# Kernel optimization log

Measured on AMD Instinct MI355X. Metric: run time of the kernel, lower is better.

Reference implementation:

```python
import jax, jax.numpy as jnp
import numpy as np

DIM = 2048
NUM_HEADS = 16
NUM_KV_HEADS = 4
HEAD_DIM = DIM // NUM_HEADS
KV_DIM = NUM_KV_HEADS * HEAD_DIM
ROPE_BASE = 10000.0
QK_GAIN_INIT = 1.0
BSZ, SEQ = 4, 2048


def rms_norm(x):
    eps = jnp.finfo(x.dtype).eps
    return x * jax.lax.rsqrt(jnp.mean(x * x, axis=-1, keepdims=True) + eps)


def rope_cos_sin(seqlen, head_dim, base, dtype):
    inv_freq = base ** (-jnp.arange(0, head_dim, 2, dtype=jnp.float32) / head_dim)
    t = jnp.arange(seqlen, dtype=jnp.float32)
    freqs = t[:, None] * inv_freq[None, :]  # [S, hd/2]
    return jnp.cos(freqs).astype(dtype), jnp.sin(freqs).astype(dtype)


def apply_rotary(x, cos, sin):
    # x: [B, H, S, hd]; cos/sin: [S, hd/2]
    x1, x2 = jnp.split(x, 2, axis=-1)
    c = cos[None, None, :, :]
    s = sin[None, None, :, :]
    return jnp.concatenate([x1 * c + x2 * s, -x1 * s + x2 * c], axis=-1)


def setup_inputs() -> dict:
    key = jax.random.key(0)
    ks = jax.random.split(key, 6)
    std = 0.02
    return {
        "x": jax.random.normal(ks[0], (BSZ, SEQ, DIM), dtype=jnp.float32),
        "Wq": jax.random.normal(ks[1], (DIM, DIM), dtype=jnp.float32) * std,
        "Wk": jax.random.normal(ks[2], (KV_DIM, DIM), dtype=jnp.float32) * std,
        "Wv": jax.random.normal(ks[3], (KV_DIM, DIM), dtype=jnp.float32) * std,
        "Wo": jax.random.normal(ks[4], (DIM, DIM), dtype=jnp.float32) * std,
        "q_gain": jnp.full((NUM_HEADS,), QK_GAIN_INIT, dtype=jnp.float32),
    }


def reference(x, Wq, Wk, Wv, Wo, q_gain):
    bsz, seqlen, dim = x.shape
    # QKV projections (F.linear: x @ W.T)
    q = (x @ Wq.T).reshape(bsz, seqlen, NUM_HEADS, HEAD_DIM).transpose(0, 2, 1, 3)
    k = (x @ Wk.T).reshape(bsz, seqlen, NUM_KV_HEADS, HEAD_DIM).transpose(0, 2, 1, 3)
    v = (x @ Wv.T).reshape(bsz, seqlen, NUM_KV_HEADS, HEAD_DIM).transpose(0, 2, 1, 3)
    # QK RMSNorm
    q = rms_norm(q)
    k = rms_norm(k)
    # RoPE
    cos, sin = rope_cos_sin(seqlen, HEAD_DIM, ROPE_BASE, q.dtype)
    q = apply_rotary(q, cos, sin)
    k = apply_rotary(k, cos, sin)
    # per-head gain
    q = q * q_gain.astype(q.dtype)[None, :, None, None]
    # GQA: repeat kv heads
    rep = NUM_HEADS // NUM_KV_HEADS
    k = jnp.repeat(k, rep, axis=1)
    v = jnp.repeat(v, rep, axis=1)
    # causal SDPA
    scale = 1.0 / jnp.sqrt(jnp.asarray(HEAD_DIM, dtype=q.dtype))
    scores = jnp.einsum("bhsd,bhtd->bhst", q, k) * scale
    causal = jnp.tril(jnp.ones((seqlen, seqlen), dtype=bool))
    scores = jnp.where(causal[None, None], scores, jnp.asarray(-jnp.inf, scores.dtype))
    attn = jax.nn.softmax(scores, axis=-1)
    y = jnp.einsum("bhst,bhtd->bhsd", attn, v)
    y = y.transpose(0, 2, 1, 3).reshape(bsz, seqlen, dim)
    return y @ Wo.T
```

## Files before the change

kernel.cpp:

```cpp
#include <hip/hip_runtime.h>
#include <hip/hip_bf16.h>

typedef __hip_bfloat16 bf16;
typedef short s16x8 __attribute__((ext_vector_type(8)));
typedef float f32x4 __attribute__((ext_vector_type(4)));

#define DIM 2048
#define NHEADS 16
#define NKVH 4
#define HD 128
#define KVDIM 512
#define BSZ 4
#define SEQ 2048
#define MROWS (BSZ*SEQ)
#define NQKV (DIM+2*KVDIM)

__device__ __forceinline__ void gld_lds16(const bf16* g, short* l) {
  __builtin_amdgcn_global_load_lds((__attribute__((address_space(1))) void*)(void*)g,
                                   (__attribute__((address_space(3))) void*)l, 16, 0, 0);
}

__global__ __launch_bounds__(256) void cast_all(
    const float* __restrict__ x,  const float* __restrict__ Wq,
    const float* __restrict__ Wk, const float* __restrict__ Wv,
    const float* __restrict__ Wo, bf16* __restrict__ xbf,
    bf16* __restrict__ Wqkv, bf16* __restrict__ Wob) {
  const int i = blockIdx.x*256 + threadIdx.x;
  const float* src; bf16* dst; int j, o;
  if (i < 2097152)      { src = x;  dst = xbf;  j = i;           o = i; }
  else if (i < 2621440) { src = Wq; dst = Wqkv; j = i - 2097152; o = i - 2097152; }
  else if (i < 2752512) { src = Wk; dst = Wqkv; j = i - 2621440; o = i - 2097152; }
  else if (i < 2883584) { src = Wv; dst = Wqkv; j = i - 2752512; o = i - 2097152; }
  else                  { src = Wo; dst = Wob;  j = i - 2883584; o = i - 2883584; }
  const float4* s4 = (const float4*)src;
  float4 a = s4[2*j];
  float4 b = s4[2*j+1];
  union { bf16 h[8]; uint4 u; } pk;
  pk.h[0] = __float2bfloat16(a.x); pk.h[1] = __float2bfloat16(a.y);
  pk.h[2] = __float2bfloat16(a.z); pk.h[3] = __float2bfloat16(a.w);
  pk.h[4] = __float2bfloat16(b.x); pk.h[5] = __float2bfloat16(b.y);
  pk.h[6] = __float2bfloat16(b.z); pk.h[7] = __float2bfloat16(b.w);
  ((uint4*)dst)[o] = pk.u;
}


template<int MQ>
__device__ __forceinline__ void lda(s16x8 (&af)[4][2], const short* pa, int rds) {
#pragma unroll
  for (int fr = 0; fr < 4; fr++)
#pragma unroll
    for (int ks = 0; ks < 2; ks++)
      af[fr][ks] = *(const s16x8*)(pa + ((MQ*4 + fr)*2 + ks)*512 + rds);
}
template<int NQ>
__device__ __forceinline__ void ldb(s16x8 (&bfv)[2][2], const short* pb, int bsub, int rds) {
#pragma unroll
  for (int fc = 0; fc < 2; fc++)
#pragma unroll
    for (int ks = 0; ks < 2; ks++)
      bfv[fc][ks] = *(const s16x8*)(pb + (bsub + (NQ*2 + fc)*2 + ks)*512 + rds);
}
template<int MQ, int NQ>
__device__ __forceinline__ void mmq(f32x4 (&acc)[8][4], const s16x8 (&af)[4][2],
                                    const s16x8 (&bfv)[2][2]) {
#pragma unroll
  for (int fr = 0; fr < 4; fr++)
#pragma unroll
    for (int fc = 0; fc < 2; fc++)
#pragma unroll
      for (int ks = 0; ks < 2; ks++)
        acc[MQ*4+fr][NQ*2+fc] = __builtin_amdgcn_mfma_f32_16x16x32_bf16(
            af[fr][ks], bfv[fc][ks], acc[MQ*4+fr][NQ*2+fc], 0, 0, 0);
}

#define WV6 asm volatile("s_waitcnt vmcnt(6)" ::: "memory")
#define WV0 asm volatile("s_waitcnt vmcnt(0)" ::: "memory")
#define WVN ((void)0)
#define GBAR __builtin_amdgcn_s_barrier()
#define WLK asm volatile("s_waitcnt lgkmcnt(0)" ::: "memory")
#define PRI1 __builtin_amdgcn_s_setprio(1)
#define PRI0 __builtin_amdgcn_s_setprio(0)

#define KT(B_, T_, S1_, S2_, WVX) do {                                          \
    const short* pa = pAr[B_];                                                  \
    const short* pb = pBr[B_];                                                  \
    s16x8 af[4][2], b0f[2][2], b1f[2][2];                                       \
                                                        \
    lda<0>(af, pa, rds); ldb<0>(b0f, pb, bsub, rds);                            \
    if (S1_) {                                                                  \
      gld_lds16(Ab +      (long)((T_)+1)*64 + eA1, &L[1-(B_)][0][4096+wid512]); \
      gld_lds16(Ab + h1 + (long)((T_)+1)*64 + eA1, &L[1-(B_)][1][4096+wid512]); \
    }                                                                           \
    GBAR; WLK; PRI1; mmq<0,0>(acc, af, b0f); PRI0; GBAR;                        \
                                                        \
    ldb<1>(b1f, pb, bsub, rds);                                                 \
    if (S2_) {                                                                  \
      gld_lds16(Ab +      (long)((T_)+2)*64 + eA0, &L[B_][0][wid512]);          \
      gld_lds16(Ab + h1 + (long)((T_)+2)*64 + eA0, &L[B_][1][wid512]);          \
    }                                                                           \
    GBAR; WLK; PRI1; mmq<0,1>(acc, af, b1f); PRI0; GBAR;                        \
                                                        \
    lda<1>(af, pa, rds);                                                        \
    if (S2_) {                                                                  \
      gld_lds16(Bb + (long)((T_)+2)*64 + eA0, &L[B_][2][wid512]);               \
      gld_lds16(Bb + (long)((T_)+2)*64 + eA1, &L[B_][2][4096+wid512]);          \
    }                                                                           \
    GBAR; WLK; PRI1; mmq<1,0>(acc, af, b0f); PRI0; GBAR;                        \
                                                        \
    if (S2_) {                                                                  \
      gld_lds16(Bb + h1 + (long)((T_)+2)*64 + eA0, &L[B_][3][wid512]);          \
      gld_lds16(Bb + h1 + (long)((T_)+2)*64 + eA1, &L[B_][3][4096+wid512]);     \
    }                                                                           \
    WVX;                                                                        \
    GBAR; PRI1; mmq<1,1>(acc, af, b1f); PRI0; GBAR;                             \
  } while (0)

template<int EPI>
__global__ __launch_bounds__(512, 2) void gemm8(
    const bf16* __restrict__ A, const bf16* __restrict__ Bm,
    float* __restrict__ Cf, bf16* __restrict__ Qo, bf16* __restrict__ Ko,
    bf16* __restrict__ Vo, int N, int K) {
  __shared__ short L[2][4][8192] __attribute__((aligned(16)));
  const int tid = threadIdx.x;
  const int lane = tid & 63, wid = tid >> 6;
  const int quad = lane >> 4, l15 = lane & 15;
  const int wm = wid >> 2, wn = wid & 3;

  const int gx  = gridDim.x;
  const int lin = blockIdx.y * gx + blockIdx.x;
  const int cpx = (gx * gridDim.y) >> 3;
  const int swz = (lin & 7) * cpx + (lin >> 3);
  const int m0 = (swz / gx) * 256, n0 = (swz % gx) * 256;

  const int rds = l15*32 + ((quad*8) ^ ((l15 & 8) << 1));
  const int bsub = (wn & 1) * 8;

  const int colx = ((lane & 3) * 8) ^ ((lane >> 5) << 4);
  const int gc   = ((wid & 1) << 5) + colx;
  const int gr0  = ((wid >> 1) << 4) + (lane >> 2);
  const long eA0 = (long)gr0 * K + gc;
  const long eA1 = eA0 + 64L * K;
  const int wid512 = wid * 512;
  const bf16* Ab = A  + (long)m0 * K;
  const bf16* Bb = Bm + (long)n0 * K;
  const long h1 = 128L * K;

  const short* pAr[2] = { &L[0][wm][0], &L[1][wm][0] };
  const short* pBr[2] = { &L[0][2 + (wn >> 1)][0], &L[1][2 + (wn >> 1)][0] };

  f32x4 acc[8][4] = {};

  gld_lds16(Ab + eA0,           &L[0][0][wid512]);
  gld_lds16(Ab + eA1,           &L[0][0][4096 + wid512]);
  gld_lds16(Ab + h1 + eA0,      &L[0][1][wid512]);
  gld_lds16(Ab + h1 + eA1,      &L[0][1][4096 + wid512]);
  gld_lds16(Bb + eA0,           &L[0][2][wid512]);
  gld_lds16(Bb + eA1,           &L[0][2][4096 + wid512]);
  gld_lds16(Bb + h1 + eA0,      &L[0][3][wid512]);
  gld_lds16(Bb + h1 + eA1,      &L[0][3][4096 + wid512]);
  gld_lds16(Ab + 64 + eA0,      &L[1][0][wid512]);
  gld_lds16(Ab + h1 + 64 + eA0, &L[1][1][wid512]);
  gld_lds16(Bb + 64 + eA0,      &L[1][2][wid512]);
  gld_lds16(Bb + 64 + eA1,      &L[1][2][4096 + wid512]);
  gld_lds16(Bb + h1 + 64 + eA0, &L[1][3][wid512]);
  gld_lds16(Bb + h1 + 64 + eA1, &L[1][3][4096 + wid512]);
  WV6;
  GBAR;

  for (int t = 0; t < 30; t += 2) {
    KT(0, t,   1, 1, WV6);
    KT(1, t+1, 1, 1, WV6);
  }
  KT(0, 30, 1, 0, WV0);
  KT(1, 31, 0, 0, WVN);

  const int colg0 = n0 + wn*64;
  const int bb = (m0 + wm*128) >> 11;
  const int sb = (m0 + wm*128) & (SEQ-1);
  if (EPI == 0) {
    float* ew = (float*)(&L[0][0][0]) + wid*4096;
    const int rowb = m0 + wm*128;
    const int rr = lane >> 3, c4 = (lane & 7)*4;
#pragma unroll
    for (int half = 0; half < 2; half++) {
#pragma unroll
      for (int mi = 0; mi < 8; mi++)
#pragma unroll
        for (int nj2 = 0; nj2 < 2; nj2++)
#pragma unroll
          for (int r = 0; r < 4; r++)
            ew[(mi*16 + quad*4 + r)*32 + nj2*16 + l15] = acc[mi][half*2 + nj2][r];
      asm volatile("" ::: "memory");
#pragma unroll
      for (int it = 0; it < 16; it++) {
        const int row = it*8 + rr;
        float4 v = *(const float4*)&ew[row*32 + c4];
        *(float4*)(Cf + (long)(rowb + row)*N + colg0 + half*32 + c4) = v;
      }
      asm volatile("" ::: "memory");
    }
  } else if (colg0 >= DIM + KVDIM) {
    const int cv = colg0 - (DIM + KVDIM);
    const int h  = cv >> 7;
    const int db = cv & 127;
    bf16* vb = Vo + ((long)(bb*NKVH + h)*HD)*SEQ + sb;
#pragma unroll
    for (int mi = 0; mi < 8; mi++)
#pragma unroll
      for (int nj = 0; nj < 4; nj++) {
        const int d = db + nj*16 + l15;
        union { bf16 h4[4]; unsigned long long u; } pk;
        pk.h4[0] = __float2bfloat16(acc[mi][nj][0]);
        pk.h4[1] = __float2bfloat16(acc[mi][nj][1]);
        pk.h4[2] = __float2bfloat16(acc[mi][nj][2]);
        pk.h4[3] = __float2bfloat16(acc[mi][nj][3]);
        *(unsigned long long*)(vb + (long)d*SEQ + mi*16 + quad*4) = pk.u;
      }
  } else {
    short* ew = &L[0][0][0] + wid*8192;
#pragma unroll
    for (int mi = 0; mi < 8; mi++)
#pragma unroll
      for (int nj = 0; nj < 4; nj++)
#pragma unroll
        for (int r = 0; r < 4; r++) {
          bf16 hv = __float2bfloat16(acc[mi][nj][r]);
          ew[(mi*16 + quad*4 + r)*64 + nj*16 + l15] = *(short*)&hv;
        }
    asm volatile("" ::: "memory");
    bf16* gb;
    if (colg0 < DIM) gb = Qo + (long)(bb*NHEADS + (colg0 >> 7))*SEQ*HD;
    else             gb = Ko + (long)(bb*NKVH + ((colg0 - DIM) >> 7))*SEQ*HD;
    const int db = colg0 & 127;
    const int rr = lane >> 3, c8 = (lane & 7)*8;
#pragma unroll
    for (int it = 0; it < 16; it++) {
      const int row = it*8 + rr;
      uint4 v = *(const uint4*)&ew[row*64 + c8];
      *(uint4*)(gb + (long)(sb + row)*HD + db + c8) = v;
    }
  }
}

__global__ __launch_bounds__(256) void norm_rope(bf16* __restrict__ Qb,
                                                 bf16* __restrict__ Kb,
                                                 const float* __restrict__ gain) {
  const int lane = threadIdx.x & 63, wid = threadIdx.x >> 6;
  const long rid = (long)blockIdx.x*4 + wid;
  const long QR = (long)BSZ*NHEADS*SEQ;
  bf16* ptr; float g; int s;
  if (rid < QR) {
    ptr = Qb + rid*HD;
    s = (int)(rid & (SEQ-1));
    const int h = (int)((rid >> 11) & 15);
    g = gain[h] * 0.08838834764831845f;
  } else {
    const long r2 = rid - QR;
    ptr = Kb + r2*HD;
    s = (int)(r2 & (SEQ-1));
    g = 1.0f;
  }
  float x1 = __bfloat162float(ptr[lane]);
  float x2 = __bfloat162float(ptr[lane+64]);
  float ss = x1*x1 + x2*x2;
#pragma unroll
  for (int off = 1; off < 64; off <<= 1) ss += __shfl_xor(ss, off);
  const float rn = rsqrtf(ss*(1.0f/128.0f) + 1.1920928955078125e-07f);
  const float inv_freq = exp2f((float)lane * -0.20762050593046014f);
  float sn, cs;
  sincosf((float)s * inv_freq, &sn, &cs);
  const float q1 = x1*rn, q2 = x2*rn;
  ptr[lane]    = __float2bfloat16((q1*cs + q2*sn)*g);
  ptr[lane+64] = __float2bfloat16((q2*cs - q1*sn)*g);
}

__global__ __launch_bounds__(256, 2) void attn(
    const bf16* __restrict__ Qb, const bf16* __restrict__ Kb,
    const bf16* __restrict__ Vtg, bf16* __restrict__ Yb) {
  __shared__ short Kt[64*136]  __attribute__((aligned(16)));
  __shared__ short Vt[128*72]  __attribute__((aligned(16)));
  __shared__ short Pt[4*2304]  __attribute__((aligned(16)));

  const int tid = threadIdx.x;
  const int lane = tid & 63, wid = tid >> 6;
  const int quad = lane >> 4, l15 = lane & 15;
  const int lin = blockIdx.y*8 + blockIdx.x;
  const int swz = (lin & 7)*64 + (lin >> 3);
  const int xb = swz & 7;
  const int bh = swz >> 3;
  const int b = bh >> 4, h = bh & 15, kvh = h >> 2;

  const bf16* kbase = Kb  + (long)(b*NKVH + kvh)*SEQ*HD;
  const bf16* vbase = Vtg + (long)(b*NKVH + kvh)*HD*SEQ;
  short* pw0 = Pt + wid*2304;
  short* pw1 = pw0 + 1152;
  const int krow = tid >> 4, kc = (tid & 15)*8;
  const int vrow = tid >> 3, vc = (tid & 7)*8;

#define LOADK(KT_) do {                                                        \
    kr0 = *(const uint4*)(kbase + (long)((KT_)*64 +  0 + krow)*HD + kc);       \
    kr1 = *(const uint4*)(kbase + (long)((KT_)*64 + 16 + krow)*HD + kc);       \
    kr2 = *(const uint4*)(kbase + (long)((KT_)*64 + 32 + krow)*HD + kc);       \
    kr3 = *(const uint4*)(kbase + (long)((KT_)*64 + 48 + krow)*HD + kc);       \
  } while (0)
#define LOADV(KT_) do {                                                        \
    vr0 = *(const uint4*)(vbase + (long)(  0 + vrow)*SEQ + (KT_)*64 + vc);     \
    vr1 = *(const uint4*)(vbase + (long)( 32 + vrow)*SEQ + (KT_)*64 + vc);     \
    vr2 = *(const uint4*)(vbase + (long)( 64 + vrow)*SEQ + (KT_)*64 + vc);     \
    vr3 = *(const uint4*)(vbase + (long)( 96 + vrow)*SEQ + (KT_)*64 + vc);     \
  } while (0)

  for (int phase = 0; phase < 2; phase++) {
    const int qt = phase ? xb : (15 - xb);
    const int q0 = qt*128 + wid*16 + l15;
    const int q1 = q0 + 64;
    const bf16* qr0 = Qb + ((long)(b*NHEADS + h)*SEQ + q0)*HD + quad*8;
    s16x8 qa0[4], qa1[4];
#pragma unroll
    for (int st = 0; st < 4; st++) {
      qa0[st] = *(const s16x8*)(qr0 + st*32);
      qa1[st] = *(const s16x8*)(qr0 + 64*HD + st*32);
    }

    f32x4 o0[8] = {}, o1[8] = {};
    float li0 = 0.0f, li1 = 0.0f;
    const int ktiles = 2*qt + 2;

    uint4 kr0, kr1, kr2, kr3, vr0, vr1, vr2, vr3;
    LOADK(0); LOADV(0);

    for (int kt = 0; kt < ktiles; kt++) {
      __syncthreads();
      *(uint4*)&Kt[( 0 + krow)*136 + kc] = kr0;
      *(uint4*)&Kt[(16 + krow)*136 + kc] = kr1;
      *(uint4*)&Kt[(32 + krow)*136 + kc] = kr2;
      *(uint4*)&Kt[(48 + krow)*136 + kc] = kr3;
      *(uint4*)&Vt[(  0 + vrow)*72 + vc] = vr0;
      *(uint4*)&Vt[( 32 + vrow)*72 + vc] = vr1;
      *(uint4*)&Vt[( 64 + vrow)*72 + vc] = vr2;
      *(uint4*)&Vt[( 96 + vrow)*72 + vc] = vr3;
      __syncthreads();
      if (kt + 1 < ktiles) { LOADK(kt+1); LOADV(kt+1); }

      f32x4 s0[4] = {}, s1[4] = {};
#pragma unroll
      for (int nt = 0; nt < 4; nt++) {
        s16x8 kf[4];
#pragma unroll
        for (int st = 0; st < 4; st++)
          kf[st] = *(const s16x8*)&Kt[(nt*16 + l15)*136 + st*32 + quad*8];
        PRI1;
#pragma unroll
        for (int st = 0; st < 4; st++) {
          s0[nt] = __builtin_amdgcn_mfma_f32_16x16x32_bf16(kf[st], qa0[st], s0[nt], 0, 0, 0);
          s1[nt] = __builtin_amdgcn_mfma_f32_16x16x32_bf16(kf[st], qa1[st], s1[nt], 0, 0, 0);
        }
        PRI0;
      }

      const bool d0 = (kt >= 2*qt);
      const bool d1 = (kt >  2*qt);
      const int tb = kt*64 + quad*4;
      union { bf16 h[16]; unsigned long long u[4]; } p0, p1;
      float rs0 = 0.0f, rs1 = 0.0f;
#pragma unroll
      for (int nt = 0; nt < 4; nt++) {
#pragma unroll
        for (int r = 0; r < 4; r++) {
          const int t = tb + nt*16 + r;
          float v0 = s0[nt][r], v1 = s1[nt][r];
          if (d0 && (t > q0)) v0 = -1e30f;
          if (d1 && (t > q1)) v1 = -1e30f;
          const float e0 = __expf(v0 - 12.0f);
          const float e1 = __expf(v1 - 12.0f);
          rs0 += e0; rs1 += e1;
          p0.h[nt*4+r] = __float2bfloat16(e0);
          p1.h[nt*4+r] = __float2bfloat16(e1);
        }
      }
      li0 += rs0; li1 += rs1;
#pragma unroll
      for (int nt = 0; nt < 4; nt++) {
        *(unsigned long long*)&pw0[l15*72 + nt*16 + quad*4] = p0.u[nt];
        *(unsigned long long*)&pw1[l15*72 + nt*16 + quad*4] = p1.u[nt];
      }

#pragma unroll
      for (int st = 0; st < 2; st++) {
        s16x8 pf0 = *(const s16x8*)&pw0[l15*72 + st*32 + quad*8];
        s16x8 pf1 = *(const s16x8*)&pw1[l15*72 + st*32 + quad*8];
        PRI1;
#pragma unroll
        for (int dt = 0; dt < 8; dt++) {
          s16x8 vf = *(const s16x8*)&Vt[(dt*16 + l15)*72 + st*32 + quad*8];
          o0[dt] = __builtin_amdgcn_mfma_f32_16x16x32_bf16(vf, pf0, o0[dt], 0, 0, 0);
          o1[dt] = __builtin_amdgcn_mfma_f32_16x16x32_bf16(vf, pf1, o1[dt], 0, 0, 0);
        }
        PRI0;
      }
    }

    li0 += __shfl_xor(li0, 16); li0 += __shfl_xor(li0, 32);
    li1 += __shfl_xor(li1, 16); li1 += __shfl_xor(li1, 32);
    const float inv0 = 1.0f / li0, inv1 = 1.0f / li1;

    short* ep = pw0;
#pragma unroll
    for (int g = 0; g < 2; g++) {
      const float inv = g ? inv1 : inv0;
      const f32x4* o = g ? o1 : o0;
      const int qg = g ? q1 : q0;
#pragma unroll
      for (int dt = 0; dt < 8; dt++) {
        union { bf16 h[4]; unsigned long long u; } pk;
        pk.h[0] = __float2bfloat16(o[dt][0]*inv);
        pk.h[1] = __float2bfloat16(o[dt][1]*inv);
        pk.h[2] = __float2bfloat16(o[dt][2]*inv);
        pk.h[3] = __float2bfloat16(o[dt][3]*inv);
        *(unsigned long long*)&ep[l15*136 + dt*16 + quad*4] = pk.u;
      }
      bf16* yb = Yb + ((long)(b*SEQ + qg - l15))*DIM + h*HD;
#pragma unroll
      for (int p = 0; p < 4; p++) {
        const int c = quad + 4*p;
        uint4 yv = *(const uint4*)&ep[l15*136 + c*8];
        *(uint4*)&yb[(long)l15*DIM + c*8] = yv;
      }
    }
  }
#undef LOADK
#undef LOADV
}

extern "C" void kernel_launch(void* const* d_in, const int* in_sizes, int n_in,
                              void* d_out, int out_size, void* d_ws, size_t ws_size,
                              hipStream_t stream) {
  (void)in_sizes; (void)n_in; (void)out_size; (void)ws_size;
  const float* x   = (const float*)d_in[0];
  const float* Wq  = (const float*)d_in[1];
  const float* Wk  = (const float*)d_in[2];
  const float* Wv  = (const float*)d_in[3];
  const float* Wo  = (const float*)d_in[4];
  const float* qg  = (const float*)d_in[5];

  char* ws = (char*)d_ws;
  bf16* xbf  = (bf16*)(ws);
  bf16* Wqkv = (bf16*)(ws + 33554432);
  bf16* Wob  = (bf16*)(ws + 46137344);
  bf16* Qb   = (bf16*)(ws + 54525952);
  bf16* Kb   = (bf16*)(ws + 88080384);
  bf16* Vb   = (bf16*)(ws + 96468992);
  bf16* Yb   = (bf16*)(ws + 104857600);

  cast_all<<<13312, 256, 0, stream>>>(x, Wq, Wk, Wv, Wo, xbf, Wqkv, Wob);

  gemm8<1><<<dim3(NQKV/256, MROWS/256), 512, 0, stream>>>(
      xbf, Wqkv, nullptr, Qb, Kb, Vb, NQKV, DIM);

  norm_rope<<<40960, 256, 0, stream>>>(Qb, Kb, qg);

  attn<<<dim3(8, BSZ*NHEADS), 256, 0, stream>>>(Qb, Kb, Vb, Yb);

  gemm8<0><<<dim3(DIM/256, MROWS/256), 512, 0, stream>>>(
      Yb, Wob, (float*)d_out, nullptr, nullptr, nullptr, DIM, DIM);
}
```

Before: 443.4 us.

## Fuse QK RMSNorm and RoPE into QKV GEMM epilogue; use nontemporal stores

Removes the separate norm_rope kernel by applying RMSNorm, rotary embedding and the per-head gain inside the QKV GEMM epilogue. Each wave stages a full 128-wide head row in shared memory and normalizes it there. This saves a full read and write pass over Q and K plus one launch. Global stores across the kernels also switch to nontemporal hints. The fused epilogue runs a serial 64-row loop with 2-byte stores and shuffle reductions per wave, which may be slow and coalesce poorly.

```diff
diff --git a/kernel.cpp b/kernel.cpp
--- a/kernel.cpp
+++ b/kernel.cpp
@@ -4,6 +4,7 @@
 typedef __hip_bfloat16 bf16;
 typedef short s16x8 __attribute__((ext_vector_type(8)));
 typedef float f32x4 __attribute__((ext_vector_type(4)));
+typedef unsigned int u32x4 __attribute__((ext_vector_type(4)));
 
 #define DIM 2048
 #define NHEADS 16
@@ -18,6 +19,21 @@
 __device__ __forceinline__ void gld_lds16(const bf16* g, short* l) {
   __builtin_amdgcn_global_load_lds((__attribute__((address_space(1))) void*)(void*)g,
                                    (__attribute__((address_space(3))) void*)l, 16, 0, 0);
+}
+
+__device__ __forceinline__ void nts16(void* p, uint4 v) {
+  u32x4 w = {v.x, v.y, v.z, v.w};
+  __builtin_nontemporal_store(w, (u32x4*)p);
+}
+__device__ __forceinline__ void nts8(void* p, unsigned long long v) {
+  __builtin_nontemporal_store(v, (unsigned long long*)p);
+}
+__device__ __forceinline__ void nts16f(void* p, float4 v) {
+  f32x4 w = {v.x, v.y, v.z, v.w};
+  __builtin_nontemporal_store(w, (f32x4*)p);
+}
+__device__ __forceinline__ void nts2(void* p, bf16 v) {
+  __builtin_nontemporal_store(*(short*)&v, (short*)p);
 }
 
 __global__ __launch_bounds__(256) void cast_all(
@@ -40,7 +56,7 @@
   pk.h[2] = __float2bfloat16(a.z); pk.h[3] = __float2bfloat16(a.w);
   pk.h[4] = __float2bfloat16(b.x); pk.h[5] = __float2bfloat16(b.y);
   pk.h[6] = __float2bfloat16(b.z); pk.h[7] = __float2bfloat16(b.w);
-  ((uint4*)dst)[o] = pk.u;
+  nts16(((uint4*)dst) + o, pk.u);
 }
 
 
@@ -119,7 +135,7 @@
 __global__ __launch_bounds__(512, 2) void gemm8(
     const bf16* __restrict__ A, const bf16* __restrict__ Bm,
     float* __restrict__ Cf, bf16* __restrict__ Qo, bf16* __restrict__ Ko,
-    bf16* __restrict__ Vo, int N, int K) {
+    bf16* __restrict__ Vo, const float* __restrict__ gain, int N, int K) {
   __shared__ short L[2][4][8192] __attribute__((aligned(16)));
   const int tid = threadIdx.x;
   const int lane = tid & 63, wid = tid >> 6;
@@ -195,11 +211,11 @@
       for (int it = 0; it < 16; it++) {
         const int row = it*8 + rr;
         float4 v = *(const float4*)&ew[row*32 + c4];
-        *(float4*)(Cf + (long)(rowb + row)*N + colg0 + half*32 + c4) = v;
+        nts16f(Cf + (long)(rowb + row)*N + colg0 + half*32 + c4, v);
       }
       asm volatile("" ::: "memory");
     }
-  } else if (colg0 >= DIM + KVDIM) {
+  } else if (n0 >= DIM + KVDIM) {
     const int cv = colg0 - (DIM + KVDIM);
     const int h  = cv >> 7;
     const int db = cv & 127;
@@ -214,10 +230,12 @@
         pk.h4[1] = __float2bfloat16(acc[mi][nj][1]);
         pk.h4[2] = __float2bfloat16(acc[mi][nj][2]);
         pk.h4[3] = __float2bfloat16(acc[mi][nj][3]);
-        *(unsigned long long*)(vb + (long)d*SEQ + mi*16 + quad*4) = pk.u;
+        nts8(vb + (long)d*SEQ + mi*16 + quad*4, pk.u);
       }
   } else {
-    short* ew = &L[0][0][0] + wid*8192;
+    short* Ls = &L[0][0][0];
+    short* rw = Ls + (wm*2 + (wn >> 1))*16384;
+    const int cw = (wn & 1)*64;
 #pragma unroll
     for (int mi = 0; mi < 8; mi++)
 #pragma unroll
@@ -225,53 +243,40 @@
 #pragma unroll
         for (int r = 0; r < 4; r++) {
           bf16 hv = __float2bfloat16(acc[mi][nj][r]);
-          ew[(mi*16 + quad*4 + r)*64 + nj*16 + l15] = *(short*)&hv;
+          rw[(mi*16 + quad*4 + r)*128 + cw + nj*16 + l15] = *(short*)&hv;
         }
-    asm volatile("" ::: "memory");
-    bf16* gb;
-    if (colg0 < DIM) gb = Qo + (long)(bb*NHEADS + (colg0 >> 7))*SEQ*HD;
-    else             gb = Ko + (long)(bb*NKVH + ((colg0 - DIM) >> 7))*SEQ*HD;
-    const int db = colg0 & 127;
-    const int rr = lane >> 3, c8 = (lane & 7)*8;
-#pragma unroll
-    for (int it = 0; it < 16; it++) {
-      const int row = it*8 + rr;
-      uint4 v = *(const uint4*)&ew[row*64 + c8];
-      *(uint4*)(gb + (long)(sb + row)*HD + db + c8) = v;
+    __syncthreads();
+    const int h2 = wn >> 1;
+    const short* rg = Ls + (wm*2 + h2)*16384;
+    const int row0 = (wn & 1)*64;
+    float g; bf16* gb;
+    if (n0 < DIM) {
+      const int h = (n0 >> 7) + h2;
+      g = gain[h] * 0.08838834764831845f;
+      gb = Qo + (long)(bb*NHEADS + h)*SEQ*HD;
+    } else {
+      const int h = ((n0 - DIM) >> 7) + h2;
+      g = 1.0f;
+      gb = Ko + (long)(bb*NKVH + h)*SEQ*HD;
+    }
+    const float inv_freq = exp2f((float)lane * -0.20762050593046014f);
+    for (int rI = 0; rI < 64; rI++) {
+      const int row = row0 + rI;
+      const float x1 = __bfloat162float(*(const bf16*)&rg[row*128 + lane]);
+      const float x2 = __bfloat162float(*(const bf16*)&rg[row*128 + 64 + lane]);
+      float ss = x1*x1 + x2*x2;
+#pragma unroll
+      for (int off = 1; off < 64; off <<= 1) ss += __shfl_xor(ss, off);
+      const float rn = rsqrtf(ss*(1.0f/128.0f) + 1.1920928955078125e-07f);
+      const int s = sb + row;
+      float sn, cs;
+      sincosf((float)s * inv_freq, &sn, &cs);
+      const float q1 = x1*rn, q2 = x2*rn;
+      bf16* pr = gb + (long)s*HD;
+      nts2(pr + lane,      __float2bfloat16((q1*cs + q2*sn)*g));
+      nts2(pr + 64 + lane, __float2bfloat16((q2*cs - q1*sn)*g));
     }
   }
-}
-
-__global__ __launch_bounds__(256) void norm_rope(bf16* __restrict__ Qb,
-                                                 bf16* __restrict__ Kb,
-                                                 const float* __restrict__ gain) {
-  const int lane = threadIdx.x & 63, wid = threadIdx.x >> 6;
-  const long rid = (long)blockIdx.x*4 + wid;
-  const long QR = (long)BSZ*NHEADS*SEQ;
-  bf16* ptr; float g; int s;
-  if (rid < QR) {
-    ptr = Qb + rid*HD;
-    s = (int)(rid & (SEQ-1));
-    const int h = (int)((rid >> 11) & 15);
-    g = gain[h] * 0.08838834764831845f;
-  } else {
-    const long r2 = rid - QR;
-    ptr = Kb + r2*HD;
-    s = (int)(r2 & (SEQ-1));
-    g = 1.0f;
-  }
-  float x1 = __bfloat162float(ptr[lane]);
-  float x2 = __bfloat162float(ptr[lane+64]);
-  float ss = x1*x1 + x2*x2;
-#pragma unroll
-  for (int off = 1; off < 64; off <<= 1) ss += __shfl_xor(ss, off);
-  const float rn = rsqrtf(ss*(1.0f/128.0f) + 1.1920928955078125e-07f);
-  const float inv_freq = exp2f((float)lane * -0.20762050593046014f);
-  float sn, cs;
-  sincosf((float)s * inv_freq, &sn, &cs);
-  const float q1 = x1*rn, q2 = x2*rn;
-  ptr[lane]    = __float2bfloat16((q1*cs + q2*sn)*g);
-  ptr[lane+64] = __float2bfloat16((q2*cs - q1*sn)*g);
 }
 
 __global__ __launch_bounds__(256, 2) void attn(
@@ -424,7 +429,7 @@
       for (int p = 0; p < 4; p++) {
         const int c = quad + 4*p;
         uint4 yv = *(const uint4*)&ep[l15*136 + c*8];
-        *(uint4*)&yb[(long)l15*DIM + c*8] = yv;
+        nts16(&yb[(long)l15*DIM + c*8], yv);
       }
     }
   }
@@ -455,12 +460,10 @@
   cast_all<<<13312, 256, 0, stream>>>(x, Wq, Wk, Wv, Wo, xbf, Wqkv, Wob);
 
   gemm8<1><<<dim3(NQKV/256, MROWS/256), 512, 0, stream>>>(
-      xbf, Wqkv, nullptr, Qb, Kb, Vb, NQKV, DIM);
-
-  norm_rope<<<40960, 256, 0, stream>>>(Qb, Kb, qg);
+      xbf, Wqkv, nullptr, Qb, Kb, Vb, qg, NQKV, DIM);
 
   attn<<<dim3(8, BSZ*NHEADS), 256, 0, stream>>>(Qb, Kb, Vb, Yb);
 
   gemm8<0><<<dim3(DIM/256, MROWS/256), 512, 0, stream>>>(
-      Yb, Wob, (float*)d_out, nullptr, nullptr, nullptr, DIM, DIM);
-}
+      Yb, Wob, (float*)d_out, nullptr, nullptr, nullptr, nullptr, DIM, DIM);
+}
```

After: 468.2 us. +5.6%, slower.
